# Kernel optimization log

Measured on AMD Instinct MI355X. Metric: run time of the kernel, lower is better.

Reference implementation:

```python
import jax, jax.numpy as jnp
import numpy as np

B, IN_DIM, D, C = 4096, 1024, 128, 10000
H, HD = 4, 32  # heads, head_dim (D = H*HD)
EXP = 4        # ffn expansion
LN_EPS = 1e-5


def _ln(x, g, b):
    m = x.mean(-1, keepdims=True)
    v = ((x - m) ** 2).mean(-1, keepdims=True)
    return (x - m) / jnp.sqrt(v + LN_EPS) * g + b


def setup_inputs() -> dict:
    key = jax.random.key(0)
    ks = jax.random.split(key, 16)
    s = 0.02
    return {
        "x": jax.random.normal(ks[0], (B, IN_DIM), jnp.float32),
        # projector
        "W1": jax.random.normal(ks[1], (IN_DIM, 2 * D), jnp.float32) * s,
        "b1": jnp.zeros((2 * D,), jnp.float32),
        "W2": jax.random.normal(ks[2], (2 * D, D), jnp.float32) * s,
        "b2": jnp.zeros((D,), jnp.float32),
        # fractal block: MHA
        "in_w": jax.random.normal(ks[3], (D, 3 * D), jnp.float32) * s,
        "in_b": jnp.zeros((3 * D,), jnp.float32),
        "out_w": jax.random.normal(ks[4], (D, D), jnp.float32) * s,
        "out_b": jnp.zeros((D,), jnp.float32),
        # fractal block: FFN
        "fw1": jax.random.normal(ks[5], (D, EXP * D), jnp.float32) * s,
        "fb1": jnp.zeros((EXP * D,), jnp.float32),
        "fw2": jax.random.normal(ks[6], (EXP * D, D), jnp.float32) * s,
        "fb2": jnp.zeros((D,), jnp.float32),
        # layernorms
        "g1": jnp.ones((D,), jnp.float32), "bt1": jnp.zeros((D,), jnp.float32),
        "g2": jnp.ones((D,), jnp.float32), "bt2": jnp.zeros((D,), jnp.float32),
        # curvature, prototypes, euclidean head
        "log_c": jnp.array(0.0, jnp.float32),  # log(1.0)
        "prototypes": jax.random.normal(ks[7], (C, D), jnp.float32) * 0.1,
        "euc_w": jax.random.normal(ks[8], (D, C), jnp.float32) * s,
        "euc_b": jnp.zeros((C,), jnp.float32),
    }


def reference(x, W1, b1, W2, b2, in_w, in_b, out_w, out_b,
              fw1, fb1, fw2, fb2, g1, bt1, g2, bt2,
              log_c, prototypes, euc_w, euc_b):
    # ---- projector MLP (exact GELU, as torch default) ----
    t = jax.nn.gelu(x @ W1 + b1, approximate=False) @ W2 + b2  # (B, D)

    # ---- FractalBlock on seq_len=1 ----
    xs = t[:, None, :]  # (B, 1, D)
    qkv = xs @ in_w + in_b  # (B, 1, 3D)
    q, k, v = jnp.split(qkv, 3, axis=-1)
    q = q.reshape(B, 1, H, HD)
    k = k.reshape(B, 1, H, HD)
    v = v.reshape(B, 1, H, HD)
    scores = jnp.einsum("bqhd,bkhd->bhqk", q, k) / jnp.sqrt(jnp.float32(HD))
    w = jax.nn.softmax(scores, axis=-1)  # seq=1 -> all ones
    attn = jnp.einsum("bhqk,bkhd->bqhd", w, v).reshape(B, 1, D)
    attn = attn @ out_w + out_b
    xs = _ln(xs + attn, g1, bt1)
    ffn = jax.nn.gelu(xs @ fw1 + fb1, approximate=False) @ fw2 + fb2
    xs = _ln(xs + ffn, g2, bt2)
    t = xs[:, 0, :]  # (B, D) tangent

    # ---- curvature ----
    c = jnp.clip(jnp.exp(log_c), 1e-4, 10.0)
    c = jnp.maximum(jnp.abs(c), 1e-6)
    sqrt_c = jnp.sqrt(c)

    # ---- exp map to Poincare ball ----
    v_norm = jnp.maximum(jnp.linalg.norm(t, axis=-1, keepdims=True), 1e-10)
    emb = jnp.tanh(sqrt_c * v_norm / 2) * t / (sqrt_c * v_norm)
    e_norm = jnp.linalg.norm(emb, axis=-1, keepdims=True)
    max_norm = (1 - 1e-5) / sqrt_c
    emb = emb * jnp.minimum(max_norm / jnp.maximum(e_norm, 1e-6), 1.0)  # (B, D)

    # ---- project prototypes inside ball ----
    p_norm = jnp.linalg.norm(prototypes, axis=-1, keepdims=True)
    protos = prototypes * jnp.minimum(max_norm / jnp.maximum(p_norm, 1e-6), 1.0)  # (C, D)

    e2 = jnp.sum(emb * emb, axis=-1)      # (B,)
    p2 = jnp.sum(protos * protos, axis=-1)  # (C,)
    diff_sq = jnp.maximum(e2[:, None] + p2[None, :] - 2.0 * emb @ protos.T, 1e-10)  # (B, C)
    denom = (1 - c * jnp.minimum(e2, 1 - 1e-5))[:, None] * (1 - c * jnp.minimum(p2, 1 - 1e-5))[None, :]
    arg = 1 + 2 * diff_sq / jnp.maximum(denom, 1e-6)
    dists = 2 / sqrt_c * jnp.arccosh(jnp.maximum(arg, 1.0 + 1e-6))  # (B, C)

    hyp_logits = -dists
    euc_logits = t @ euc_w + euc_b
    return hyp_logits, euc_logits, emb
```

## Files before the change

### kernel.cpp

```cpp
#include <hip/hip_runtime.h>
#include <cmath>


using bf16x8 = __attribute__((ext_vector_type(8))) __bf16;
using f32x4  = __attribute__((ext_vector_type(4))) float;

#define DEVINL __device__ __forceinline__

DEVINL unsigned short f2b(float f) {
    unsigned int u = __builtin_bit_cast(unsigned int, f);
    u = (u + 0x7fffu + ((u >> 16) & 1u)) >> 16;
    return (unsigned short)u;
}

DEVINL float gelu_exact(float x) {
    return 0.5f * x * (1.0f + erff(x * 0.70710678118654752440f));
}

DEVINL float get_c(const float* logc) {
    float c = expf(logc[0]);
    c = fminf(fmaxf(c, 1e-4f), 10.0f);
    return fmaxf(fabsf(c), 1e-6f);
}

DEVINL void async16(const unsigned short* g, unsigned short* l) {
    __builtin_amdgcn_global_load_lds(
        (const __attribute__((address_space(1))) void*)g,
        (__attribute__((address_space(3))) void*)l, 16, 0, 0);
}


DEVINL void t_cvt(const float* __restrict__ src, unsigned short* __restrict__ dst,
                  int K, int N, int Npad, int ld, int off, int tblk, int tid,
                  float tile[32][33]) {
    int kbCount = K >> 5;
    int kb = (tblk % kbCount) * 32, nb = (tblk / kbCount) * 32;
    int tx = tid & 31, ty = tid >> 5;
    #pragma unroll
    for (int i = 0; i < 32; i += 8) {
        int k = kb + ty + i, n = nb + tx;
        tile[ty + i][tx] = (k < K && n < N) ? src[(size_t)k * ld + off + n] : 0.0f;
    }
    __syncthreads();
    #pragma unroll
    for (int i = 0; i < 32; i += 8) {
        int n = nb + ty + i, k = kb + tx;
        if (n < Npad && k < K) dst[(size_t)n * K + k] = f2b(tile[tx][ty + i]);
    }
}

#define PB0 4096
#define PB1 (PB0 + 256)
#define PB2 (PB1 + 64)
#define PB3 (PB2 + 64)
#define PB4 (PB3 + 1264)
#define PB5 (PB4 + 2528)

__global__ void k_prep(const float* __restrict__ x, const float* __restrict__ W1,
                       const float* __restrict__ fw1, const float* __restrict__ fw2,
                       const float* __restrict__ euc_w, const float* __restrict__ P,
                       const float* __restrict__ logc,
                       unsigned short* __restrict__ xbf, unsigned short* __restrict__ W1T,
                       unsigned short* __restrict__ FW1T, unsigned short* __restrict__ FW2T,
                       unsigned short* __restrict__ EUCWT, unsigned short* __restrict__ PROTB,
                       float* __restrict__ p2a, float* __restrict__ dpa) {
    __shared__ float tile[32][33];
    int b = blockIdx.x, tid = threadIdx.x;
    if (b < PB0) {
        int i = b * 256 + tid;
        float4 v = ((const float4*)x)[i];
        ushort4 o;
        o.x = f2b(v.x); o.y = f2b(v.y); o.z = f2b(v.z); o.w = f2b(v.w);
        ((ushort4*)xbf)[i] = o;
    } else if (b < PB1) {
        t_cvt(W1, W1T, 1024, 256, 256, 256, 0, b - PB0, tid, tile);
    } else if (b < PB2) {
        t_cvt(fw1, FW1T, 128, 512, 512, 512, 0, b - PB1, tid, tile);
    } else if (b < PB3) {
        t_cvt(fw2, FW2T, 512, 128, 128, 128, 0, b - PB2, tid, tile);
    } else if (b < PB4) {
        t_cvt(euc_w, EUCWT, 128, 10000, 10112, 10000, 0, b - PB3, tid, tile);
    } else {
        int lane = tid & 63;
        int row = (b - PB4) * 4 + (tid >> 6);
        size_t base = (size_t)row * 128;
        if (row < 10000) {
            float a = P[base + lane], bb = P[base + 64 + lane];
            float n2 = a * a + bb * bb;
            #pragma unroll
            for (int m = 32; m > 0; m >>= 1) n2 += __shfl_xor(n2, m, 64);
            float c = get_c(logc);
            float sq = sqrtf(c);
            float mx = (1.0f - 1e-5f) / sq;
            float pn = sqrtf(n2);
            float f = fminf(mx / fmaxf(pn, 1e-6f), 1.0f);
            a *= f; bb *= f;
            PROTB[base + lane] = f2b(a); PROTB[base + 64 + lane] = f2b(bb);
            if (lane == 0) {
                float p2 = n2 * f * f;
                p2a[row] = p2;
                dpa[row] = 1.0f - c * fminf(p2, 1.0f - 1e-5f);
            }
        } else if (row < 10112) {
            PROTB[base + lane] = 0; PROTB[base + 64 + lane] = 0;
            if (lane == 0) { p2a[row] = 0.0f; dpa[row] = 1.0f; }
        }
    }
}

__global__ void k_fold(const float* __restrict__ in_w, const float* __restrict__ in_b,
                       const float* __restrict__ out_w, const float* __restrict__ out_b,
                       const float* __restrict__ W2, const float* __restrict__ b2,
                       unsigned short* __restrict__ W2ppT, float* __restrict__ bpp) {
    __shared__ float WoCol[128];
    __shared__ float WcCol[128];
    const int n = blockIdx.x, t = threadIdx.x;
    WoCol[t] = out_w[t * 128 + n];
    __syncthreads();
    float a = (t == n) ? 1.0f : 0.0f;
    for (int j = 0; j < 128; j++) a += in_w[t * 384 + 256 + j] * WoCol[j];
    WcCol[t] = a;
    __syncthreads();
    #pragma unroll
    for (int h = 0; h < 2; h++) {
        int k = t + h * 128;
        float s = 0.f;
        for (int j = 0; j < 128; j++) s += W2[k * 128 + j] * WcCol[j];
        W2ppT[n * 256 + k] = f2b(s);
    }
    if (t == 0) {
        float s = 0.f;
        for (int j = 0; j < 128; j++) s += b2[j] * WcCol[j];
        float s2 = 0.f;
        for (int j = 0; j < 128; j++) s2 += in_b[256 + j] * WoCol[j];
        bpp[n] = s + s2 + out_b[n];
    }
}

#define EP_GELU 0
#define EP_LN1 1
#define EP_LN2HYP 2

template <int EP, int BK>
__global__ __launch_bounds__(256) void k_gemm(
    const unsigned short* __restrict__ A, const unsigned short* __restrict__ Bm,
    const float* __restrict__ bias, int K, int Nstore,
    float* __restrict__ outF, unsigned short* __restrict__ outH,
    const float* __restrict__ g, const float* __restrict__ bt,
    const float* __restrict__ resF, const float* __restrict__ logc,
    float* __restrict__ embF, unsigned short* __restrict__ embH,
    float* __restrict__ e2a, float* __restrict__ dea) {
    __shared__ __align__(16) unsigned short As[128 * BK];
    __shared__ __align__(16) unsigned short Bs[128 * BK];
    const int tid = threadIdx.x, lane = tid & 63, wid = tid >> 6;
    const int row0 = blockIdx.x * 128, col0 = blockIdx.y * 128;
    const int q = lane >> 4, l16 = lane & 15;
    const int wm = (wid >> 1) * 64, wn = (wid & 1) * 64;
    const int sw = (l16 & 7) * 8;
    constexpr int CPR = BK / 8;
    constexpr int ITER = 128 * CPR / 256;

    f32x4 acc[4][4];
    #pragma unroll
    for (int i = 0; i < 4; i++)
        #pragma unroll
        for (int j = 0; j < 4; j++) acc[i][j] = {0.f, 0.f, 0.f, 0.f};

    for (int k0 = 0; k0 < K; k0 += BK) {
        #pragma unroll
        for (int it = 0; it < ITER; ++it) {
            int idx = it * 256 + tid;
            int r = idx / CPR, ck = (idx % CPR) * 8;
            int cks = ck ^ ((r & 7) * 8);
            async16(&A[(size_t)(row0 + r) * K + k0 + cks], &As[idx * 8]);
        }
        #pragma unroll
        for (int it = 0; it < ITER; ++it) {
            int idx = it * 256 + tid;
            int r = idx / CPR, ck = (idx % CPR) * 8;
            int cks = ck ^ ((r & 7) * 8);
            async16(&Bm[(size_t)(col0 + r) * K + k0 + cks], &Bs[idx * 8]);
        }
        __syncthreads();
        #pragma unroll
        for (int kk = 0; kk < BK; kk += 32) {
            bf16x8 af[4], bfr[4];
            #pragma unroll
            for (int i = 0; i < 4; i++)
                af[i] = *(const bf16x8*)&As[(wm + i * 16 + l16) * BK + ((kk + q * 8) ^ sw)];
            #pragma unroll
            for (int j = 0; j < 4; j++)
                bfr[j] = *(const bf16x8*)&Bs[(wn + j * 16 + l16) * BK + ((kk + q * 8) ^ sw)];
            #pragma unroll
            for (int i = 0; i < 4; i++)
                #pragma unroll
                for (int j = 0; j < 4; j++)
                    acc[i][j] = __builtin_amdgcn_mfma_f32_16x16x32_bf16(
                        af[i], bfr[j], acc[i][j], 0, 0, 0);
        }
        __syncthreads();
    }

    if (EP == EP_GELU) {
        #pragma unroll
        for (int j = 0; j < 4; j++) {
            int col = col0 + wn + j * 16 + l16;
            float bb = bias[col];
            #pragma unroll
            for (int i = 0; i < 4; i++)
                #pragma unroll
                for (int rg = 0; rg < 4; rg++) {
                    int row = row0 + wm + i * 16 + q * 4 + rg;
                    outH[(size_t)row * Nstore + col] = f2b(gelu_exact(acc[i][j][rg] + bb));
                }
        }
        return;
    }

    #pragma unroll
    for (int j = 0; j < 4; j++) {
        int col = wn + j * 16 + l16;
        float bb = bias[col];
        #pragma unroll
        for (int i = 0; i < 4; i++)
            #pragma unroll
            for (int rg = 0; rg < 4; rg++) {
                int rl = wm + i * 16 + q * 4 + rg;
                float v = acc[i][j][rg] + bb;
                if (EP == EP_LN2HYP) v += resF[(size_t)(row0 + rl) * 128 + col];
                acc[i][j][rg] = v;
            }
    }
    float* sred = (float*)As;
    #pragma unroll
    for (int i = 0; i < 4; i++)
        #pragma unroll
        for (int rg = 0; rg < 4; rg++) {
            float s = 0.f, ss = 0.f;
            #pragma unroll
            for (int j = 0; j < 4; j++) { float v = acc[i][j][rg]; s += v; ss += v * v; }
            #pragma unroll
            for (int m = 1; m < 16; m <<= 1) {
                s += __shfl_xor(s, m, 64); ss += __shfl_xor(ss, m, 64);
            }
            if (l16 == 0) {
                int rl = wm + i * 16 + q * 4 + rg;
                sred[rl * 4 + (wid & 1) * 2] = s;
                sred[rl * 4 + (wid & 1) * 2 + 1] = ss;
            }
        }
    __syncthreads();

    float c = 0.f, sq = 0.f, mx = 0.f;
    if (EP == EP_LN2HYP) { c = get_c(logc); sq = sqrtf(c); mx = (1.0f - 1e-5f) / sq; }

    #pragma unroll
    for (int i = 0; i < 4; i++)
        #pragma unroll
        for (int rg = 0; rg < 4; rg++) {
            int rl = wm + i * 16 + q * 4 + rg;
            int row = row0 + rl;
            float sum = sred[rl * 4 + 0] + sred[rl * 4 + 2];
            float sqs = sred[rl * 4 + 1] + sred[rl * 4 + 3];
            float m = sum * (1.0f / 128.0f);
            float var = sqs * (1.0f / 128.0f) - m * m;
            float inv = rsqrtf(var + 1e-5f);
            #pragma unroll
            for (int j = 0; j < 4; j++) {
                int col = wn + j * 16 + l16;
                float y = (acc[i][j][rg] - m) * inv * g[col] + bt[col];
                acc[i][j][rg] = y;
                if (EP == EP_LN1) {
                    outF[(size_t)row * 128 + col] = y;
                    outH[(size_t)row * 128 + col] = f2b(y);
                } else {
                    outH[(size_t)row * 128 + col] = f2b(y);
                }
            }
        }

    if (EP == EP_LN2HYP) {
        float* sred2 = (float*)Bs;
        #pragma unroll
        for (int i = 0; i < 4; i++)
            #pragma unroll
            for (int rg = 0; rg < 4; rg++) {
                float s2 = 0.f;
                #pragma unroll
                for (int j = 0; j < 4; j++) { float y = acc[i][j][rg]; s2 += y * y; }
                #pragma unroll
                for (int m = 1; m < 16; m <<= 1) s2 += __shfl_xor(s2, m, 64);
                if (l16 == 0) {
                    int rl = wm + i * 16 + q * 4 + rg;
                    sred2[rl * 2 + (wid & 1)] = s2;
                }
            }
        __syncthreads();
        #pragma unroll
        for (int i = 0; i < 4; i++)
            #pragma unroll
            for (int rg = 0; rg < 4; rg++) {
                int rl = wm + i * 16 + q * 4 + rg;
                int row = row0 + rl;
                float vn2 = sred2[rl * 2] + sred2[rl * 2 + 1];
                float vn = fmaxf(sqrtf(vn2), 1e-10f);
                float sc = tanhf(0.5f * sq * vn) / (sq * vn);
                float en2 = sc * sc * vn2;
                float en = sqrtf(en2);
                float f = fminf(mx / fmaxf(en, 1e-6f), 1.0f);
                float scale = sc * f;
                float e2v = en2 * f * f;
                #pragma unroll
                for (int j = 0; j < 4; j++) {
                    int col = wn + j * 16 + l16;
                    float e = acc[i][j][rg] * scale;
                    embF[(size_t)row * 128 + col] = e;
                    embH[(size_t)row * 128 + col] = f2b(e);
                }
                if (l16 == 0 && (wid & 1) == 0) {
                    e2a[row] = e2v;
                    dea[row] = 1.0f - c * fminf(e2v, 1.0f - 1e-5f);
                }
            }
    }
}

__global__ __launch_bounds__(256) void k_heads(
    const unsigned short* __restrict__ embH, const unsigned short* __restrict__ tH,
    const unsigned short* __restrict__ protB, const unsigned short* __restrict__ eucWT,
    const float* __restrict__ e2a, const float* __restrict__ dea,
    const float* __restrict__ p2a, const float* __restrict__ dpa,
    const float* __restrict__ euc_b, const float* __restrict__ logc,
    float* __restrict__ outHyp, float* __restrict__ outEuc) {
    __shared__ __align__(16) unsigned short S[4096 * 8];
    const bool hyp = blockIdx.y < 79;
    const int cb = hyp ? blockIdx.y : blockIdx.y - 79;
    const unsigned short* Ap = hyp ? embH : tH;
    const unsigned short* Bp = hyp ? protB : eucWT;
    const int tid = threadIdx.x, lane = tid & 63, wid = tid >> 6;
    const int row0 = blockIdx.x * 128, col0 = cb * 128;
    const int q = lane >> 4, l16 = lane & 15;
    const int wm = (wid >> 1) * 64, wn = (wid & 1) * 64;
    const int sw = (l16 & 7) * 8;

    #pragma unroll
    for (int it = 0; it < 16; ++it) {
        int idx = it * 256 + tid;
        if (idx < 2048) {
            int r = idx >> 4, ck = (idx & 15) * 8;
            int cks = ck ^ ((r & 7) * 8);
            async16(&Ap[(size_t)(row0 + r) * 128 + cks], &S[idx * 8]);
        } else {
            int idb = idx - 2048;
            int r = idb >> 4, ck = (idb & 15) * 8;
            int cks = ck ^ ((r & 7) * 8);
            async16(&Bp[(size_t)(col0 + r) * 128 + cks], &S[idx * 8]);
        }
    }
    __syncthreads();
    const unsigned short* As = S;
    const unsigned short* Bs = S + 2048 * 8;

    f32x4 acc[4][4];
    #pragma unroll
    for (int i = 0; i < 4; i++)
        #pragma unroll
        for (int j = 0; j < 4; j++) acc[i][j] = {0.f, 0.f, 0.f, 0.f};
    #pragma unroll
    for (int kk = 0; kk < 128; kk += 32) {
        bf16x8 af[4], bfr[4];
        #pragma unroll
        for (int i = 0; i < 4; i++)
            af[i] = *(const bf16x8*)&As[(wm + i * 16 + l16) * 128 + ((kk + q * 8) ^ sw)];
        #pragma unroll
        for (int j = 0; j < 4; j++)
            bfr[j] = *(const bf16x8*)&Bs[(wn + j * 16 + l16) * 128 + ((kk + q * 8) ^ sw)];
        #pragma unroll
        for (int i = 0; i < 4; i++)
            #pragma unroll
            for (int j = 0; j < 4; j++)
                acc[i][j] = __builtin_amdgcn_mfma_f32_16x16x32_bf16(
                    af[i], bfr[j], acc[i][j], 0, 0, 0);
    }

    if (hyp) {
        float c = get_c(logc);
        float invsq = 2.0f / sqrtf(c);
        #pragma unroll
        for (int j = 0; j < 4; j++) {
            int col = col0 + wn + j * 16 + l16;
            if (col < 10000) {
                float p2v = p2a[col], dpv = dpa[col];
                #pragma unroll
                for (int i = 0; i < 4; i++)
                    #pragma unroll
                    for (int rg = 0; rg < 4; rg++) {
                        int row = row0 + wm + i * 16 + q * 4 + rg;
                        float v = acc[i][j][rg];
                        float diff = fmaxf(e2a[row] + p2v - 2.0f * v, 1e-10f);
                        float den = fmaxf(dea[row] * dpv, 1e-6f);
                        float arg = fmaxf(1.0f + 2.0f * diff / den, 1.0f + 1e-6f);
                        float d = __logf(arg + sqrtf(arg * arg - 1.0f));
                        outHyp[(size_t)row * 10000 + col] = -invsq * d;
                    }
            }
        }
    } else {
        #pragma unroll
        for (int j = 0; j < 4; j++) {
            int col = col0 + wn + j * 16 + l16;
            if (col < 10000) {
                float bb = euc_b[col];
                #pragma unroll
                for (int i = 0; i < 4; i++)
                    #pragma unroll
                    for (int rg = 0; rg < 4; rg++) {
                        int row = row0 + wm + i * 16 + q * 4 + rg;
                        outEuc[(size_t)row * 10000 + col] = acc[i][j][rg] + bb;
                    }
            }
        }
    }
}


extern "C" void kernel_launch(void* const* d_in, const int* in_sizes, int n_in,
                              void* d_out, int out_size, void* d_ws, size_t ws_size,
                              hipStream_t stream) {
    const float* x      = (const float*)d_in[0];
    const float* W1     = (const float*)d_in[1];
    const float* b1     = (const float*)d_in[2];
    const float* W2     = (const float*)d_in[3];
    const float* b2     = (const float*)d_in[4];
    const float* in_w   = (const float*)d_in[5];
    const float* in_b   = (const float*)d_in[6];
    const float* out_w  = (const float*)d_in[7];
    const float* out_b  = (const float*)d_in[8];
    const float* fw1    = (const float*)d_in[9];
    const float* fb1    = (const float*)d_in[10];
    const float* fw2    = (const float*)d_in[11];
    const float* fb2    = (const float*)d_in[12];
    const float* g1     = (const float*)d_in[13];
    const float* bt1    = (const float*)d_in[14];
    const float* g2     = (const float*)d_in[15];
    const float* bt2    = (const float*)d_in[16];
    const float* logc   = (const float*)d_in[17];
    const float* protos = (const float*)d_in[18];
    const float* euc_w  = (const float*)d_in[19];
    const float* euc_b  = (const float*)d_in[20];

    float* out_hyp = (float*)d_out;
    float* out_euc = out_hyp + (size_t)4096 * 10000;
    float* out_emb = out_euc + (size_t)4096 * 10000;

    constexpr size_t O_XBF   = 0;
    constexpr size_t O_W1T   = O_XBF   + (size_t)4096 * 1024 * 2;
    constexpr size_t O_FW1T  = O_W1T   + (size_t)256 * 1024 * 2;
    constexpr size_t O_FW2T  = O_FW1T  + (size_t)512 * 128 * 2;
    constexpr size_t O_EUCWT = O_FW2T  + (size_t)128 * 512 * 2;
    constexpr size_t O_PROTB = O_EUCWT + (size_t)10112 * 128 * 2;
    constexpr size_t O_W2PP  = O_PROTB + (size_t)10112 * 128 * 2;
    constexpr size_t O_BPP   = O_W2PP  + (size_t)128 * 256 * 2;
    constexpr size_t O_HBF   = O_BPP   + (size_t)128 * 4;
    constexpr size_t O_XS1F  = O_HBF   + (size_t)4096 * 256 * 2;
    constexpr size_t O_XS1B  = O_XS1F  + (size_t)4096 * 128 * 4;
    constexpr size_t O_FHB   = O_XS1B  + (size_t)4096 * 128 * 2;
    constexpr size_t O_TFB   = O_FHB   + (size_t)4096 * 512 * 2;
    constexpr size_t O_EMBB  = O_TFB   + (size_t)4096 * 128 * 2;
    constexpr size_t O_E2    = O_EMBB  + (size_t)4096 * 128 * 2;
    constexpr size_t O_DE    = O_E2    + (size_t)4096 * 4;
    constexpr size_t O_P2    = O_DE    + (size_t)4096 * 4;
    constexpr size_t O_DP    = O_P2    + (size_t)10112 * 4;

    char* w = (char*)d_ws;
    auto US = [&](size_t o) { return (unsigned short*)(w + o); };
    auto FP = [&](size_t o) { return (float*)(w + o); };

    k_prep<<<PB5, 256, 0, stream>>>(x, W1, fw1, fw2, euc_w, protos, logc,
                                    US(O_XBF), US(O_W1T), US(O_FW1T), US(O_FW2T),
                                    US(O_EUCWT), US(O_PROTB), FP(O_P2), FP(O_DP));
    k_fold<<<128, 128, 0, stream>>>(in_w, in_b, out_w, out_b, W2, b2,
                                    US(O_W2PP), FP(O_BPP));

    k_gemm<EP_GELU, 64><<<dim3(32, 2), 256, 0, stream>>>(
        US(O_XBF), US(O_W1T), b1, 1024, 256, nullptr, US(O_HBF),
        nullptr, nullptr, nullptr, nullptr, nullptr, nullptr, nullptr, nullptr);
    k_gemm<EP_LN1, 64><<<dim3(32, 1), 256, 0, stream>>>(
        US(O_HBF), US(O_W2PP), FP(O_BPP), 256, 128, FP(O_XS1F), US(O_XS1B),
        g1, bt1, nullptr, nullptr, nullptr, nullptr, nullptr, nullptr);
    k_gemm<EP_GELU, 128><<<dim3(32, 4), 256, 0, stream>>>(
        US(O_XS1B), US(O_FW1T), fb1, 128, 512, nullptr, US(O_FHB),
        nullptr, nullptr, nullptr, nullptr, nullptr, nullptr, nullptr, nullptr);
    k_gemm<EP_LN2HYP, 64><<<dim3(32, 1), 256, 0, stream>>>(
        US(O_FHB), US(O_FW2T), fb2, 512, 128, nullptr, US(O_TFB),
        g2, bt2, FP(O_XS1F), logc, out_emb, US(O_EMBB), FP(O_E2), FP(O_DE));
    k_heads<<<dim3(32, 158), 256, 0, stream>>>(
        US(O_EMBB), US(O_TFB), US(O_PROTB), US(O_EUCWT),
        FP(O_E2), FP(O_DE), FP(O_P2), FP(O_DP), euc_b, logc, out_hyp, out_euc);
}
```

Measured before the change: 584.3 us.

## Make k_heads persistent over column tiles with double-buffered B staging

```diff
diff --git a/kernel.cpp b/kernel.cpp
--- a/kernel.cpp
+++ b/kernel.cpp
@@ -42,10 +42,16 @@
         tile[ty + i][tx] = (k < K && n < N) ? src[(size_t)k * ld + off + n] : 0.0f;
     }
     __syncthreads();
-    #pragma unroll
-    for (int i = 0; i < 32; i += 8) {
-        int n = nb + ty + i, k = kb + tx;
-        if (n < Npad && k < K) dst[(size_t)n * K + k] = f2b(tile[tx][ty + i]);
+    int tx2 = (tid & 15) * 2, ty2 = tid >> 4;
+    #pragma unroll
+    for (int i = 0; i < 32; i += 16) {
+        int n = nb + ty2 + i, k = kb + tx2;
+        if (n < Npad && k + 1 < K + 1) {
+            ushort2 o2;
+            o2.x = f2b(tile[tx2][ty2 + i]);
+            o2.y = f2b(tile[tx2 + 1][ty2 + i]);
+            *(ushort2*)&dst[(size_t)n * K + k] = o2;
+        }
     }
 }
 
@@ -325,101 +331,133 @@
     }
 }
 
-__global__ __launch_bounds__(256) void k_heads(
+__global__ __launch_bounds__(256, 2) void k_heads(
     const unsigned short* __restrict__ embH, const unsigned short* __restrict__ tH,
     const unsigned short* __restrict__ protB, const unsigned short* __restrict__ eucWT,
     const float* __restrict__ e2a, const float* __restrict__ dea,
     const float* __restrict__ p2a, const float* __restrict__ dpa,
     const float* __restrict__ euc_b, const float* __restrict__ logc,
     float* __restrict__ outHyp, float* __restrict__ outEuc) {
-    __shared__ __align__(16) unsigned short S[4096 * 8];
-    const bool hyp = blockIdx.y < 79;
-    const int cb = hyp ? blockIdx.y : blockIdx.y - 79;
-    const unsigned short* Ap = hyp ? embH : tH;
-    const unsigned short* Bp = hyp ? protB : eucWT;
+    __shared__ __align__(16) unsigned short Bs[2][128 * 128];
     const int tid = threadIdx.x, lane = tid & 63, wid = tid >> 6;
-    const int row0 = blockIdx.x * 128, col0 = cb * 128;
+    const int row0 = blockIdx.x * 128, g = blockIdx.y;
     const int q = lane >> 4, l16 = lane & 15;
     const int wm = (wid >> 1) * 64, wn = (wid & 1) * 64;
     const int sw = (l16 & 7) * 8;
-
-    #pragma unroll
-    for (int it = 0; it < 16; ++it) {
-        int idx = it * 256 + tid;
-        if (idx < 2048) {
+    const int nh = (94 - g) >> 4;
+    const int nt = 2 * nh;
+
+    auto stageB = [&](int buf, int ti) {
+        const unsigned short* Bp = (ti < nh) ? protB : eucWT;
+        const int cb = (ti < nh) ? (g + 16 * ti) : (g + 16 * (ti - nh));
+        const size_t c0 = (size_t)cb * 128;
+        __builtin_amdgcn_sched_barrier(0);
+        #pragma unroll
+        for (int it = 0; it < 8; ++it) {
+            int idx = it * 256 + tid;
             int r = idx >> 4, ck = (idx & 15) * 8;
             int cks = ck ^ ((r & 7) * 8);
-            async16(&Ap[(size_t)(row0 + r) * 128 + cks], &S[idx * 8]);
-        } else {
-            int idb = idx - 2048;
-            int r = idb >> 4, ck = (idb & 15) * 8;
-            int cks = ck ^ ((r & 7) * 8);
-            async16(&Bp[(size_t)(col0 + r) * 128 + cks], &S[idx * 8]);
-        }
-    }
-    __syncthreads();
-    const unsigned short* As = S;
-    const unsigned short* Bs = S + 2048 * 8;
-
-    f32x4 acc[4][4];
+            async16(&Bp[(c0 + r) * 128 + cks], &Bs[buf][idx * 8]);
+        }
+        __builtin_amdgcn_sched_barrier(0);
+    };
+
+    bf16x8 af[4][4];
+    auto loadA = [&](const unsigned short* Ap) {
+        #pragma unroll
+        for (int i = 0; i < 4; i++)
+            #pragma unroll
+            for (int ks = 0; ks < 4; ks++)
+                af[i][ks] = *(const bf16x8*)&Ap[
+                    (size_t)(row0 + wm + i * 16 + l16) * 128 + ks * 32 + q * 8];
+    };
+
+    stageB(0, 0);
+    loadA(embH);
+    float e2r[4][4], der[4][4];
     #pragma unroll
     for (int i = 0; i < 4; i++)
         #pragma unroll
-        for (int j = 0; j < 4; j++) acc[i][j] = {0.f, 0.f, 0.f, 0.f};
-    #pragma unroll
-    for (int kk = 0; kk < 128; kk += 32) {
-        bf16x8 af[4], bfr[4];
+        for (int rg = 0; rg < 4; rg++) {
+            int row = row0 + wm + i * 16 + q * 4 + rg;
+            e2r[i][rg] = e2a[row];
+            der[i][rg] = dea[row];
+        }
+    const float c = get_c(logc);
+    const float kmul = -2.0f / sqrtf(c);
+    asm volatile("s_waitcnt vmcnt(0)" ::: "memory");
+    __builtin_amdgcn_s_barrier();
+    __builtin_amdgcn_sched_barrier(0);
+
+    bool prev_partial = false;
+    for (int ti = 0; ti < nt; ++ti) {
+        if (ti > 0) {
+            if (prev_partial) asm volatile("s_waitcnt vmcnt(0)" ::: "memory");
+            else              asm volatile("s_waitcnt vmcnt(32)" ::: "memory");
+            __builtin_amdgcn_s_barrier();
+            __builtin_amdgcn_sched_barrier(0);
+        }
+        const bool isHyp = ti < nh;
+        const int cb = isHyp ? (g + 16 * ti) : (g + 16 * (ti - nh));
+        const int c0 = cb * 128;
+        if (ti == nh) loadA(tH);
+
+        float pv[4], dv[4], bb[4];
+        #pragma unroll
+        for (int j = 0; j < 4; j++) {
+            int col = c0 + wn + j * 16 + l16;
+            if (isHyp) { pv[j] = p2a[col]; dv[j] = dpa[col]; }
+            else       { bb[j] = (col < 10000) ? euc_b[col] : 0.0f; }
+        }
+
+        const int cur = ti & 1;
+        f32x4 acc[4][4];
         #pragma unroll
         for (int i = 0; i < 4; i++)
-            af[i] = *(const bf16x8*)&As[(wm + i * 16 + l16) * 128 + ((kk + q * 8) ^ sw)];
-        #pragma unroll
-        for (int j = 0; j < 4; j++)
-            bfr[j] = *(const bf16x8*)&Bs[(wn + j * 16 + l16) * 128 + ((kk + q * 8) ^ sw)];
-        #pragma unroll
-        for (int i = 0; i < 4; i++)
+            #pragma unroll
+            for (int j = 0; j < 4; j++) acc[i][j] = {0.f, 0.f, 0.f, 0.f};
+        #pragma unroll
+        for (int ks = 0; ks < 4; ks++) {
+            bf16x8 bfr[4];
             #pragma unroll
             for (int j = 0; j < 4; j++)
-                acc[i][j] = __builtin_amdgcn_mfma_f32_16x16x32_bf16(
-                    af[i], bfr[j], acc[i][j], 0, 0, 0);
-    }
-
-    if (hyp) {
-        float c = get_c(logc);
-        float invsq = 2.0f / sqrtf(c);
-        #pragma unroll
-        for (int j = 0; j < 4; j++) {
-            int col = col0 + wn + j * 16 + l16;
-            if (col < 10000) {
-                float p2v = p2a[col], dpv = dpa[col];
-                #pragma unroll
-                for (int i = 0; i < 4; i++)
-                    #pragma unroll
-                    for (int rg = 0; rg < 4; rg++) {
-                        int row = row0 + wm + i * 16 + q * 4 + rg;
-                        float v = acc[i][j][rg];
-                        float diff = fmaxf(e2a[row] + p2v - 2.0f * v, 1e-10f);
-                        float den = fmaxf(dea[row] * dpv, 1e-6f);
-                        float arg = fmaxf(1.0f + 2.0f * diff / den, 1.0f + 1e-6f);
-                        float d = __logf(arg + sqrtf(arg * arg - 1.0f));
-                        outHyp[(size_t)row * 10000 + col] = -invsq * d;
+                bfr[j] = *(const bf16x8*)&Bs[cur][
+                    (wn + j * 16 + l16) * 128 + ((ks * 32 + q * 8) ^ sw)];
+            #pragma unroll
+            for (int i = 0; i < 4; i++)
+                #pragma unroll
+                for (int j = 0; j < 4; j++)
+                    acc[i][j] = __builtin_amdgcn_mfma_f32_16x16x32_bf16(
+                        af[i][ks], bfr[j], acc[i][j], 0, 0, 0);
+        }
+
+        auto epi = [&](int i) {
+            #pragma unroll
+            for (int rg = 0; rg < 4; rg++) {
+                int row = row0 + wm + i * 16 + q * 4 + rg;
+                #pragma unroll
+                for (int j = 0; j < 4; j++) {
+                    int col = c0 + wn + j * 16 + l16;
+                    float v = acc[i][j][rg];
+                    if (isHyp) {
+                        float diff = fmaxf(fmaf(-2.0f, v, e2r[i][rg] + pv[j]), 1e-10f);
+                        float den = fmaxf(der[i][rg] * dv[j], 1e-6f);
+                        float arg = fmaf(2.0f * diff, __builtin_amdgcn_rcpf(den), 1.0f);
+                        arg = fmaxf(arg, 1.0f + 1e-6f);
+                        float t = __builtin_amdgcn_sqrtf(fmaf(arg, arg, -1.0f));
+                        if (col < 10000)
+                            outHyp[(size_t)row * 10000 + col] = kmul * __logf(arg + t);
+                    } else {
+                        if (col < 10000)
+                            outEuc[(size_t)row * 10000 + col] = v + bb[j];
                     }
-            }
-        }
-    } else {
-        #pragma unroll
-        for (int j = 0; j < 4; j++) {
-            int col = col0 + wn + j * 16 + l16;
-            if (col < 10000) {
-                float bb = euc_b[col];
-                #pragma unroll
-                for (int i = 0; i < 4; i++)
-                    #pragma unroll
-                    for (int rg = 0; rg < 4; rg++) {
-                        int row = row0 + wm + i * 16 + q * 4 + rg;
-                        outEuc[(size_t)row * 10000 + col] = acc[i][j][rg] + bb;
-                    }
-            }
-        }
+                }
+            }
+        };
+        epi(0); epi(1);
+        if (ti + 1 < nt) stageB(cur ^ 1, ti + 1);
+        epi(2); epi(3);
+        prev_partial = (c0 == 9984);
     }
 }
 
@@ -494,7 +532,7 @@
     k_gemm<EP_LN2HYP, 64><<<dim3(32, 1), 256, 0, stream>>>(
         US(O_FHB), US(O_FW2T), fb2, 512, 128, nullptr, US(O_TFB),
         g2, bt2, FP(O_XS1F), logc, out_emb, US(O_EMBB), FP(O_E2), FP(O_DE));
-    k_heads<<<dim3(32, 158), 256, 0, stream>>>(
+    k_heads<<<dim3(32, 16), 256, 0, stream>>>(
         US(O_EMBB), US(O_TFB), US(O_PROTB), US(O_EUCWT),
         FP(O_E2), FP(O_DE), FP(O_P2), FP(O_DP), euc_b, logc, out_hyp, out_euc);
 }
```

New measurement: 597.7 us. 2.3% more time.

## Load A fragments directly from global in heads kernel, halve LDS, reorder epilogue

Applied to the files above, without the earlier changes.

```diff
diff --git a/kernel.cpp b/kernel.cpp
--- a/kernel.cpp
+++ b/kernel.cpp
@@ -42,10 +42,16 @@
         tile[ty + i][tx] = (k < K && n < N) ? src[(size_t)k * ld + off + n] : 0.0f;
     }
     __syncthreads();
-    #pragma unroll
-    for (int i = 0; i < 32; i += 8) {
-        int n = nb + ty + i, k = kb + tx;
-        if (n < Npad && k < K) dst[(size_t)n * K + k] = f2b(tile[tx][ty + i]);
+    int tx2 = (tid & 15) * 2, ty2 = tid >> 4;
+    #pragma unroll
+    for (int i = 0; i < 32; i += 16) {
+        int n = nb + ty2 + i, k = kb + tx2;
+        if (n < Npad) {
+            ushort2 o2;
+            o2.x = f2b(tile[tx2][ty2 + i]);
+            o2.y = f2b(tile[tx2 + 1][ty2 + i]);
+            *(ushort2*)&dst[(size_t)n * K + k] = o2;
+        }
     }
 }
 
@@ -325,101 +331,110 @@
     }
 }
 
-__global__ __launch_bounds__(256) void k_heads(
+__global__ __launch_bounds__(256, 4) void k_heads(
     const unsigned short* __restrict__ embH, const unsigned short* __restrict__ tH,
     const unsigned short* __restrict__ protB, const unsigned short* __restrict__ eucWT,
     const float* __restrict__ e2a, const float* __restrict__ dea,
     const float* __restrict__ p2a, const float* __restrict__ dpa,
     const float* __restrict__ euc_b, const float* __restrict__ logc,
     float* __restrict__ outHyp, float* __restrict__ outEuc) {
-    __shared__ __align__(16) unsigned short S[4096 * 8];
+    __shared__ __align__(16) unsigned short Bs[128 * 128];
     const bool hyp = blockIdx.y < 79;
     const int cb = hyp ? blockIdx.y : blockIdx.y - 79;
     const unsigned short* Ap = hyp ? embH : tH;
     const unsigned short* Bp = hyp ? protB : eucWT;
     const int tid = threadIdx.x, lane = tid & 63, wid = tid >> 6;
-    const int row0 = blockIdx.x * 128, col0 = cb * 128;
+    const int row0 = blockIdx.x * 128, c0 = cb * 128;
     const int q = lane >> 4, l16 = lane & 15;
     const int wm = (wid >> 1) * 64, wn = (wid & 1) * 64;
     const int sw = (l16 & 7) * 8;
 
     #pragma unroll
-    for (int it = 0; it < 16; ++it) {
+    for (int it = 0; it < 8; ++it) {
         int idx = it * 256 + tid;
-        if (idx < 2048) {
-            int r = idx >> 4, ck = (idx & 15) * 8;
-            int cks = ck ^ ((r & 7) * 8);
-            async16(&Ap[(size_t)(row0 + r) * 128 + cks], &S[idx * 8]);
-        } else {
-            int idb = idx - 2048;
-            int r = idb >> 4, ck = (idb & 15) * 8;
-            int cks = ck ^ ((r & 7) * 8);
-            async16(&Bp[(size_t)(col0 + r) * 128 + cks], &S[idx * 8]);
-        }
+        int r = idx >> 4, ck = (idx & 15) * 8;
+        int cks = ck ^ ((r & 7) * 8);
+        async16(&Bp[(size_t)(c0 + r) * 128 + cks], &Bs[idx * 8]);
     }
     __syncthreads();
-    const unsigned short* As = S;
-    const unsigned short* Bs = S + 2048 * 8;
 
     f32x4 acc[4][4];
     #pragma unroll
     for (int i = 0; i < 4; i++)
         #pragma unroll
         for (int j = 0; j < 4; j++) acc[i][j] = {0.f, 0.f, 0.f, 0.f};
-    #pragma unroll
-    for (int kk = 0; kk < 128; kk += 32) {
-        bf16x8 af[4], bfr[4];
-        #pragma unroll
-        for (int i = 0; i < 4; i++)
-            af[i] = *(const bf16x8*)&As[(wm + i * 16 + l16) * 128 + ((kk + q * 8) ^ sw)];
-        #pragma unroll
-        for (int j = 0; j < 4; j++)
-            bfr[j] = *(const bf16x8*)&Bs[(wn + j * 16 + l16) * 128 + ((kk + q * 8) ^ sw)];
-        #pragma unroll
-        for (int i = 0; i < 4; i++)
-            #pragma unroll
-            for (int j = 0; j < 4; j++)
+
+    const size_t arow = (size_t)(row0 + wm + l16) * 128 + q * 8;
+    #pragma unroll
+    for (int ks = 0; ks < 4; ks++) {
+        bf16x8 af[4];
+        #pragma unroll
+        for (int i = 0; i < 4; i++)
+            af[i] = *(const bf16x8*)&Ap[arow + (size_t)i * 16 * 128 + ks * 32];
+        #pragma unroll
+        for (int j = 0; j < 4; j++) {
+            bf16x8 b8 = *(const bf16x8*)&Bs[
+                (wn + j * 16 + l16) * 128 + ((ks * 32 + q * 8) ^ sw)];
+            #pragma unroll
+            for (int i = 0; i < 4; i++)
                 acc[i][j] = __builtin_amdgcn_mfma_f32_16x16x32_bf16(
-                    af[i], bfr[j], acc[i][j], 0, 0, 0);
+                    af[i], b8, acc[i][j], 0, 0, 0);
+        }
     }
 
     if (hyp) {
-        float c = get_c(logc);
-        float invsq = 2.0f / sqrtf(c);
+        const float c = get_c(logc);
+        const float kmul = -2.0f / sqrtf(c);
+        float pv[4], dv[4], e2r[4][4], der[4][4];
         #pragma unroll
         for (int j = 0; j < 4; j++) {
-            int col = col0 + wn + j * 16 + l16;
-            if (col < 10000) {
-                float p2v = p2a[col], dpv = dpa[col];
-                #pragma unroll
-                for (int i = 0; i < 4; i++)
-                    #pragma unroll
-                    for (int rg = 0; rg < 4; rg++) {
-                        int row = row0 + wm + i * 16 + q * 4 + rg;
-                        float v = acc[i][j][rg];
-                        float diff = fmaxf(e2a[row] + p2v - 2.0f * v, 1e-10f);
-                        float den = fmaxf(dea[row] * dpv, 1e-6f);
-                        float arg = fmaxf(1.0f + 2.0f * diff / den, 1.0f + 1e-6f);
-                        float d = __logf(arg + sqrtf(arg * arg - 1.0f));
-                        outHyp[(size_t)row * 10000 + col] = -invsq * d;
-                    }
-            }
-        }
+            int col = c0 + wn + j * 16 + l16;
+            pv[j] = p2a[col]; dv[j] = dpa[col];
+        }
+        #pragma unroll
+        for (int i = 0; i < 4; i++)
+            #pragma unroll
+            for (int rg = 0; rg < 4; rg++) {
+                int row = row0 + wm + i * 16 + q * 4 + rg;
+                e2r[i][rg] = e2a[row]; der[i][rg] = dea[row];
+            }
+        #pragma unroll
+        for (int i = 0; i < 4; i++)
+            #pragma unroll
+            for (int rg = 0; rg < 4; rg++) {
+                int row = row0 + wm + i * 16 + q * 4 + rg;
+                #pragma unroll
+                for (int j = 0; j < 4; j++) {
+                    int col = c0 + wn + j * 16 + l16;
+                    float v = acc[i][j][rg];
+                    float diff = fmaxf(fmaf(-2.0f, v, e2r[i][rg] + pv[j]), 1e-10f);
+                    float den = fmaxf(der[i][rg] * dv[j], 1e-6f);
+                    float arg = fmaf(2.0f * diff, __builtin_amdgcn_rcpf(den), 1.0f);
+                    arg = fmaxf(arg, 1.0f + 1e-6f);
+                    float t = __builtin_amdgcn_sqrtf(fmaf(arg, arg, -1.0f));
+                    if (col < 10000)
+                        outHyp[(size_t)row * 10000 + col] = kmul * __logf(arg + t);
+                }
+            }
     } else {
+        float bb[4];
         #pragma unroll
         for (int j = 0; j < 4; j++) {
-            int col = col0 + wn + j * 16 + l16;
-            if (col < 10000) {
-                float bb = euc_b[col];
-                #pragma unroll
-                for (int i = 0; i < 4; i++)
-                    #pragma unroll
-                    for (int rg = 0; rg < 4; rg++) {
-                        int row = row0 + wm + i * 16 + q * 4 + rg;
-                        outEuc[(size_t)row * 10000 + col] = acc[i][j][rg] + bb;
-                    }
-            }
-        }
+            int col = c0 + wn + j * 16 + l16;
+            bb[j] = (col < 10000) ? euc_b[col] : 0.0f;
+        }
+        #pragma unroll
+        for (int i = 0; i < 4; i++)
+            #pragma unroll
+            for (int rg = 0; rg < 4; rg++) {
+                int row = row0 + wm + i * 16 + q * 4 + rg;
+                #pragma unroll
+                for (int j = 0; j < 4; j++) {
+                    int col = c0 + wn + j * 16 + l16;
+                    if (col < 10000)
+                        outEuc[(size_t)row * 10000 + col] = acc[i][j][rg] + bb[j];
+                }
+            }
     }
 }
 
```

After: 548.2 us. 1.07x faster.
